# Performance work log

Measured on AMD Instinct MI355X. Metric: run time of the kernel, lower is better.

The kernel has to match this reference:

```python
import jax, jax.numpy as jnp
import numpy as np
from jax import lax

B, N, IN_DIM, OUT_DIM = 4, 8192, 32, 128
NPOINT, RADIUS, NSAMPLE = 1024, 0.2, 32
BN_EPS = 1e-5

def _sqdist(a, b):
    # a: [B,n,3], b: [B,m,3] -> [B,n,m] squared euclidean distances
    return (jnp.sum(a * a, -1)[:, :, None] + jnp.sum(b * b, -1)[:, None, :]
            - 2.0 * jnp.einsum('bnd,bmd->bnm', a, b))

def _fps(xyz, npoint):
    # farthest point sampling, sequential by nature -> lax.scan over npoint steps
    Bn, Np, _ = xyz.shape
    def step(carry, _):
        dist, far = carry
        centroid = jnp.take_along_axis(xyz, far[:, None, None], axis=1)  # [B,1,3]
        dist = jnp.minimum(dist, jnp.sum((xyz - centroid) ** 2, -1))
        return (dist, jnp.argmax(dist, -1).astype(jnp.int32)), far
    init = (jnp.full((Bn, Np), 1e10, xyz.dtype), jnp.zeros((Bn,), jnp.int32))
    _, idx = lax.scan(step, init, None, length=npoint)
    return idx.T  # [B, npoint]

def _gather_points(x, idx):  # x [B,N,D], idx [B,...] -> [B,...,D]
    return jax.vmap(lambda p, i: p[i])(x, idx)

def _gather_feats(f, idx):  # f [B,C,N], idx [B,...] -> [B,C,...]
    return jax.vmap(lambda p, i: p[:, i])(f, idx)

def _ball_query(new_xyz, xyz):
    d2 = _sqdist(new_xyz, xyz)  # [B,P,N]
    Np = xyz.shape[1]
    cand = jnp.where(d2 < RADIUS ** 2, jnp.arange(Np, dtype=jnp.int32), Np)
    idx = -lax.top_k(-cand, NSAMPLE)[0]  # first NSAMPLE in-radius indices (sorted)
    return jnp.where(idx == Np, idx[..., :1], idx)  # pad misses with first hit

def _bn(x, gamma, beta, axes):
    # training-mode batch norm over `axes`, channel axis = 1
    m = jnp.mean(x, axes, keepdims=True)
    v = jnp.var(x, axes, keepdims=True)
    sh = (1, -1) + (1,) * (x.ndim - 2)
    return (x - m) * (gamma.reshape(sh) / jnp.sqrt(v + BN_EPS)) + beta.reshape(sh)

def _forward(xyz, features, W_sa0, g_sa0, b_sa0, W_sa1, g_sa1, b_sa1, W_sa2, g_sa2, b_sa2,
             W_fp0, g_fp0, b_fp0, W_fp1, g_fp1, b_fp1,
             Wc1, bc1, g1, b1, Wc2, bc2, g2, b2, Wc3, bc3):
    # --- PointnetSAModuleVotes: FPS + ball query + group (use_xyz, normalize_xyz) + MLP + maxpool ---
    fps_idx = _fps(xyz, NPOINT)
    new_xyz = _gather_points(xyz, fps_idx)                           # [B,P,3]
    gidx = _ball_query(new_xyz, xyz)                                 # [B,P,S]
    gxyz = (_gather_points(xyz, gidx) - new_xyz[:, :, None, :]) / RADIUS  # centered, normalized
    h = jnp.concatenate([gxyz.transpose(0, 3, 1, 2), _gather_feats(features, gidx)], 1)  # [B,3+C,P,S]
    for W, g, b in ((W_sa0, g_sa0, b_sa0), (W_sa1, g_sa1, b_sa1), (W_sa2, g_sa2, b_sa2)):
        h = jax.nn.relu(_bn(jnp.einsum('oc,bcps->bops', W, h), g, b, (0, 2, 3)))
    feat_sa = jnp.max(h, -1)                                         # [B,128,P]
    # --- PointnetFPModule: 3-NN interpolation (inv-sq-dist weights) + skip concat + MLP ---
    d2 = _sqdist(xyz, new_xyz)                                       # [B,N,P]
    neg, idx3 = lax.top_k(-d2, 3)
    recip = 1.0 / (jnp.maximum(-neg, 0.0) + 1e-8)
    w = recip / jnp.sum(recip, -1, keepdims=True)                    # [B,N,3]
    interp = jnp.sum(_gather_feats(feat_sa, idx3) * w[:, None, :, :], -1)  # [B,128,N]
    h = jnp.concatenate([interp, features], 1)                       # [B,128+C,N]
    for W, g, b in ((W_fp0, g_fp0, b_fp0), (W_fp1, g_fp1, b_fp1)):
        h = jax.nn.relu(_bn(jnp.einsum('oc,bcn->bon', W, h), g, b, (0, 2)))
    seed_features = h                                                # [B,128,N]
    # --- vote head: conv1d(1) + BN + ReLU x2, then conv1d(1) -> [3 offset | 1 score | out_dim feat] ---
    net = jax.nn.relu(_bn(jnp.einsum('oc,bcn->bon', Wc1, seed_features) + bc1[:, None], g1, b1, (0, 2)))
    net = jax.nn.relu(_bn(jnp.einsum('oc,bcn->bon', Wc2, net) + bc2[:, None], g2, b2, (0, 2)))
    net = (jnp.einsum('oc,bcn->bon', Wc3, net) + bc3[:, None]).transpose(0, 2, 1)  # [B,N,4+out]
    offset = net[:, :, 0:3]
    vote_xyz = xyz + offset
    vote_scores = jax.nn.sigmoid(net[:, :, 3])
    vf = seed_features.transpose(0, 2, 1) + net[:, :, 4:]
    vote_features = vf / jnp.maximum(jnp.linalg.norm(vf, axis=2, keepdims=True), 1e-12)  # F.normalize
    return vote_xyz, offset, vote_scores, vote_features

def setup_inputs():
    key = jax.random.key(0)
    ks = jax.random.split(key, 40)
    he = lambda k, o, c: jax.random.normal(k, (o, c), jnp.float32) * float(np.sqrt(2.0 / c))
    inp = {'xyz': jax.random.uniform(ks[0], (B, N, 3), jnp.float32),
           'features': jax.random.normal(ks[1], (B, IN_DIM, N), jnp.float32)}
    j = 2
    dims_sa = [IN_DIM + 3, 128, 128, 128]  # use_xyz adds 3 to first layer
    for i in range(3):
        inp[f'W_sa{i}'] = he(ks[j], 128, dims_sa[i]); j += 1
        inp[f'g_sa{i}'] = 1.0 + 0.1 * jax.random.normal(ks[j], (128,), jnp.float32); j += 1
        inp[f'b_sa{i}'] = 0.1 * jax.random.normal(ks[j], (128,), jnp.float32); j += 1
    dims_fp = [IN_DIM + 128, 128, 128]
    for i in range(2):
        inp[f'W_fp{i}'] = he(ks[j], 128, dims_fp[i]); j += 1
        inp[f'g_fp{i}'] = 1.0 + 0.1 * jax.random.normal(ks[j], (128,), jnp.float32); j += 1
        inp[f'b_fp{i}'] = 0.1 * jax.random.normal(ks[j], (128,), jnp.float32); j += 1
    inp['Wc1'] = he(ks[j], 128, 128); j += 1
    inp['bc1'] = 0.01 * jax.random.normal(ks[j], (128,), jnp.float32); j += 1
    inp['g1'] = 1.0 + 0.1 * jax.random.normal(ks[j], (128,), jnp.float32); j += 1
    inp['b1'] = 0.1 * jax.random.normal(ks[j], (128,), jnp.float32); j += 1
    inp['Wc2'] = he(ks[j], 128, 128); j += 1
    inp['bc2'] = 0.01 * jax.random.normal(ks[j], (128,), jnp.float32); j += 1
    inp['g2'] = 1.0 + 0.1 * jax.random.normal(ks[j], (128,), jnp.float32); j += 1
    inp['b2'] = 0.1 * jax.random.normal(ks[j], (128,), jnp.float32); j += 1
    inp['Wc3'] = he(ks[j], 4 + OUT_DIM, 128); j += 1
    inp['bc3'] = 0.01 * jax.random.normal(ks[j], (4 + OUT_DIM,), jnp.float32); j += 1
    return inp

def reference(xyz, features, W_sa0, g_sa0, b_sa0, W_sa1, g_sa1, b_sa1, W_sa2, g_sa2, b_sa2,
              W_fp0, g_fp0, b_fp0, W_fp1, g_fp1, b_fp1,
              Wc1, bc1, g1, b1, Wc2, bc2, g2, b2, Wc3, bc3):
    return _forward(xyz, features, W_sa0, g_sa0, b_sa0, W_sa1, g_sa1, b_sa1, W_sa2, g_sa2, b_sa2,
                    W_fp0, g_fp0, b_fp0, W_fp1, g_fp1, b_fp1,
                    Wc1, bc1, g1, b1, Wc2, bc2, g2, b2, Wc3, bc3)
```

## Files before the change

kernel.cpp:

```cpp
#include <hip/hip_runtime.h>
#include <hip/hip_bf16.h>
#include <math.h>

namespace {

constexpr int BB  = 4;
constexpr int NN  = 8192;
constexpr int IND = 32;
constexpr int NPT = 1024;
constexpr int NSM = 32;
constexpr int SACOLS = BB * NPT * NSM;
constexpr int FPCOLS = BB * NN;
constexpr int CSTR = 132;

__device__ __forceinline__ double sqn3_f64(float x, float y, float z) {
#pragma clang fp contract(off)
    double dx = (double)x, dy = (double)y, dz = (double)z;
    return (dx * dx + dy * dy) + dz * dz;
}
__device__ __forceinline__ double dot3_f64(float ax, float ay, float az,
                                           float bx, float by, float bz) {
#pragma clang fp contract(off)
    return ((double)ax * (double)bx + (double)ay * (double)by) + (double)az * (double)bz;
}
__device__ __forceinline__ double sqd_f64(double sa, double sb, double dot) {
#pragma clang fp contract(off)
    return (sa + sb) - 2.0 * dot;
}

__global__ __launch_bounds__(256)
void k_fps(const float* __restrict__ xyz, float* __restrict__ new_xyz)
{
#pragma clang fp contract(off)
    const int b   = blockIdx.x;
    const int tid = threadIdx.x;
    const float* P = xyz + (size_t)b * NN * 3;

    __shared__ float sx[NN];
    __shared__ float sy[NN];
    __shared__ float sz[NN];
    __shared__ float ctrs[NPT * 3];
    __shared__ unsigned long long wv[2][4];

    float px[32], py[32], pz[32], dd[32];
#pragma unroll
    for (int i = 0; i < 32; ++i) {
        int p = tid + i * 256;
        float x = P[p * 3 + 0], y = P[p * 3 + 1], z = P[p * 3 + 2];
        px[i] = x; py[i] = y; pz[i] = z; dd[i] = 1e10f;
        sx[p] = x; sy[p] = y; sz[p] = z;
    }
    float cx = P[0], cy = P[1], cz = P[2];
    __syncthreads();

    for (int t = 0; t < NPT; ++t) {
        if (tid == 0) {
            ctrs[t * 3 + 0] = cx;
            ctrs[t * 3 + 1] = cy;
            ctrs[t * 3 + 2] = cz;
        }
        if (t == NPT - 1) break;

        unsigned long long best = 0ull;
#pragma unroll
        for (int i = 0; i < 32; ++i) {
            float dx = px[i] - cx;
            float dy = py[i] - cy;
            float dz = pz[i] - cz;
            float d  = (dx * dx + dy * dy) + dz * dz;
            float nd = fminf(dd[i], d);
            dd[i] = nd;
            unsigned int lo = (unsigned)(NN - 1) - (unsigned)(tid + i * 256);
            unsigned long long cand =
                ((unsigned long long)__float_as_uint(nd) << 32) | lo;
            best = (cand > best) ? cand : best;
        }
        for (int off = 32; off > 0; off >>= 1) {
            unsigned long long o = __shfl_down(best, off);
            best = (o > best) ? o : best;
        }
        const int buf = t & 1;
        if ((tid & 63) == 0) wv[buf][tid >> 6] = best;
        __syncthreads();
        unsigned long long w0 = wv[buf][0];
#pragma unroll
        for (int k = 1; k < 4; ++k) {
            unsigned long long wk = wv[buf][k];
            w0 = (wk > w0) ? wk : w0;
        }
        const int idx = (NN - 1) - (int)(unsigned)(w0 & 0xFFFFFFFFull);
        cx = sx[idx]; cy = sy[idx]; cz = sz[idx];
    }

    __syncthreads();
    float* O = new_xyz + (size_t)b * NPT * 3;
    for (int i = tid; i < NPT * 3; i += 256) O[i] = ctrs[i];
}

__global__ __launch_bounds__(256)
void k_ballquery(const float* __restrict__ xyz, const float* __restrict__ new_xyz,
                 int* __restrict__ gidx)
{
    const int wv   = threadIdx.x >> 6;
    const int lane = threadIdx.x & 63;
    const int cid  = blockIdx.x * 4 + wv;
    const int b    = cid >> 10;
    const float* P = xyz + (size_t)b * NN * 3;

    const float cx = new_xyz[(size_t)cid * 3 + 0];
    const float cy = new_xyz[(size_t)cid * 3 + 1];
    const float cz = new_xyz[(size_t)cid * 3 + 2];
    const double sa = sqn3_f64(cx, cy, cz);
    const double R2 = 0.2 * 0.2;

    int cnt = 0;
    int firstidx = -1;
    int* G = gidx + (size_t)cid * NSM;

    for (int base = 0; base < NN && cnt < NSM; base += 64) {
        int p = base + lane;
        float x = P[p * 3 + 0], y = P[p * 3 + 1], z = P[p * 3 + 2];
        double sb  = sqn3_f64(x, y, z);
        double dot = dot3_f64(cx, cy, cz, x, y, z);
        double d2  = sqd_f64(sa, sb, dot);
        bool hit = d2 < R2;
        unsigned long long m = __ballot(hit);
        if (firstidx < 0 && m != 0ull) firstidx = base + __builtin_ctzll(m);
        int before = __popcll(m & ((1ull << lane) - 1ull));
        int pos = cnt + before;
        if (hit && pos < NSM) G[pos] = p;
        cnt += __popcll(m);
    }
    if (firstidx < 0) firstidx = 0;
    if (cnt < NSM) {
        for (int j = cnt + lane; j < NSM; j += 64) G[j] = firstidx;
    }
}

__global__ __launch_bounds__(256)
void k_group(const float* __restrict__ xyz, const float* __restrict__ feats,
             const float* __restrict__ new_xyz, const int* __restrict__ gidx,
             float* __restrict__ h0)
{
    const int col = blockIdx.x * 256 + threadIdx.x;
    const int cid = col >> 5;
    const int b   = col >> 15;
    const int g   = gidx[col];
    const float* Pt = xyz + ((size_t)b * NN + g) * 3;
    const float* Ct = new_xyz + (size_t)cid * 3;
    h0[(size_t)0 * SACOLS + col] = __fsub_rn(Pt[0], Ct[0]) / 0.2f;
    h0[(size_t)1 * SACOLS + col] = __fsub_rn(Pt[1], Ct[1]) / 0.2f;
    h0[(size_t)2 * SACOLS + col] = __fsub_rn(Pt[2], Ct[2]) / 0.2f;
    const float* FT = feats + (size_t)b * IND * NN;
    for (int c = 0; c < IND; ++c)
        h0[(size_t)(3 + c) * SACOLS + col] = FT[(size_t)c * NN + g];
}

__global__ __launch_bounds__(256)
void k_conv(const float* __restrict__ X, const float* __restrict__ W,
            const float* __restrict__ bias,
            const float* __restrict__ scale, const float* __restrict__ shift,
            float* __restrict__ Z, int Cin, int Cout, int ncol, int apply_act)
{
    __shared__ __align__(16) float Xs[32][64];
    __shared__ float Ws[64][33];
    const int tid  = threadIdx.x;
    const int col0 = blockIdx.x * 64;
    const int o0   = blockIdx.y * 64;
    const int tx   = tid & 15;
    const int ty   = tid >> 4;
    float acc[4][4] = {};

    for (int kk = 0; kk < Cin; kk += 32) {
#pragma unroll
        for (int i = 0; i < 8; ++i) {
            int idx = tid + i * 256;
            int c = idx >> 6, cc = idx & 63;
            int ch = kk + c;
            float v = 0.0f;
            if (ch < Cin) {
                v = X[(size_t)ch * ncol + col0 + cc];
                if (apply_act) v = fmaxf(fmaf(v, scale[ch], shift[ch]), 0.0f);
            }
            Xs[c][cc] = v;
        }
#pragma unroll
        for (int i = 0; i < 8; ++i) {
            int idx = tid + i * 256;
            int o = idx >> 5, c = idx & 31;
            int ch = kk + c, oo = o0 + o;
            Ws[o][c] = (ch < Cin && oo < Cout) ? W[(size_t)oo * Cin + ch] : 0.0f;
        }
        __syncthreads();
#pragma unroll
        for (int c = 0; c < 32; ++c) {
            const float4 xv = *reinterpret_cast<const float4*>(&Xs[c][tx * 4]);
            float w0 = Ws[ty * 4 + 0][c];
            float w1 = Ws[ty * 4 + 1][c];
            float w2 = Ws[ty * 4 + 2][c];
            float w3 = Ws[ty * 4 + 3][c];
            acc[0][0] = fmaf(w0, xv.x, acc[0][0]); acc[0][1] = fmaf(w0, xv.y, acc[0][1]);
            acc[0][2] = fmaf(w0, xv.z, acc[0][2]); acc[0][3] = fmaf(w0, xv.w, acc[0][3]);
            acc[1][0] = fmaf(w1, xv.x, acc[1][0]); acc[1][1] = fmaf(w1, xv.y, acc[1][1]);
            acc[1][2] = fmaf(w1, xv.z, acc[1][2]); acc[1][3] = fmaf(w1, xv.w, acc[1][3]);
            acc[2][0] = fmaf(w2, xv.x, acc[2][0]); acc[2][1] = fmaf(w2, xv.y, acc[2][1]);
            acc[2][2] = fmaf(w2, xv.z, acc[2][2]); acc[2][3] = fmaf(w2, xv.w, acc[2][3]);
            acc[3][0] = fmaf(w3, xv.x, acc[3][0]); acc[3][1] = fmaf(w3, xv.y, acc[3][1]);
            acc[3][2] = fmaf(w3, xv.z, acc[3][2]); acc[3][3] = fmaf(w3, xv.w, acc[3][3]);
        }
        __syncthreads();
    }
#pragma unroll
    for (int i = 0; i < 4; ++i) {
        int o = o0 + ty * 4 + i;
        if (o >= Cout) break;
        float bz = bias ? bias[o] : 0.0f;
#pragma unroll
        for (int j = 0; j < 4; ++j)
            Z[(size_t)o * ncol + col0 + tx * 4 + j] = acc[i][j] + bz;
    }
}

__global__ __launch_bounds__(256)
void k_stats_partial(const float* __restrict__ Z, double* __restrict__ part, int ncol, int nb)
{
    const int c = blockIdx.x, blk = blockIdx.y;
    const int chunk = ncol / nb;
    const float* p = Z + (size_t)c * ncol + (size_t)blk * chunk;
    double s = 0.0, q = 0.0;
    for (int j = threadIdx.x; j < chunk; j += 256) { double v = (double)p[j]; s += v; q += v * v; }
    __shared__ double ss[256];
    __shared__ double qq[256];
    ss[threadIdx.x] = s; qq[threadIdx.x] = q;
    __syncthreads();
    for (int off = 128; off > 0; off >>= 1) {
        if (threadIdx.x < off) { ss[threadIdx.x] += ss[threadIdx.x + off]; qq[threadIdx.x] += qq[threadIdx.x + off]; }
        __syncthreads();
    }
    if (threadIdx.x == 0) {
        part[(size_t)(c * nb + blk) * 2 + 0] = ss[0];
        part[(size_t)(c * nb + blk) * 2 + 1] = qq[0];
    }
}

__global__ void k_stats_final(const double* __restrict__ part,
                              const float* __restrict__ gamma, const float* __restrict__ beta,
                              float* __restrict__ sc_out, float* __restrict__ sh_out,
                              int C, int nb, double n)
{
    int c = threadIdx.x;
    if (c >= C) return;
    double s = 0.0, q = 0.0;
    for (int i = 0; i < nb; ++i) {
        s += part[(size_t)(c * nb + i) * 2 + 0];
        q += part[(size_t)(c * nb + i) * 2 + 1];
    }
    double mean = s / n;
    double var  = q / n - mean * mean;
    double scl  = (double)gamma[c] / sqrt(var + 1e-5);
    sc_out[c] = (float)scl;
    sh_out[c] = (float)((double)beta[c] - mean * scl);
}

__global__ __launch_bounds__(256)
void k_maxpool(const float* __restrict__ Z, const float* __restrict__ sc,
               const float* __restrict__ sh, float* __restrict__ feat)
{
    const int idx = blockIdx.x * 256 + threadIdx.x;
    const int bp  = idx & 4095;
    const int c   = idx >> 12;
    const float s = sc[c], h = sh[c];
    const float* p = Z + (size_t)c * SACOLS + (size_t)bp * 32;
    float m = 0.0f;
    for (int ss = 0; ss < 32; ++ss) m = fmaxf(m, fmaxf(fmaf(p[ss], s, h), 0.0f));
    feat[(size_t)c * (BB * NPT) + bp] = m;
}

__global__ __launch_bounds__(256)
void k_3nn(const float* __restrict__ xyz, const float* __restrict__ new_xyz,
           int* __restrict__ idx3, float* __restrict__ w3)
{
    const int gid = blockIdx.x * 256 + threadIdx.x;
    const int b = gid >> 13;
    __shared__ float  cxs[NPT];
    __shared__ float  cys[NPT];
    __shared__ float  czs[NPT];
    __shared__ double cns[NPT];
    const float* C = new_xyz + (size_t)b * NPT * 3;
    for (int i = threadIdx.x; i < NPT; i += 256) {
        float x = C[i * 3], y = C[i * 3 + 1], z = C[i * 3 + 2];
        cxs[i] = x; cys[i] = y; czs[i] = z; cns[i] = sqn3_f64(x, y, z);
    }
    __syncthreads();

    const float* P = xyz + (size_t)gid * 3;
    const float px = P[0], py = P[1], pz = P[2];
    const double sb = sqn3_f64(px, py, pz);
    double d0 = 1e30, d1 = 1e30, d2v = 1e30;
    int    i0 = 0, i1 = 0, i2 = 0;
    for (int m = 0; m < NPT; ++m) {
        double dot = dot3_f64(px, py, pz, cxs[m], cys[m], czs[m]);
        double d   = sqd_f64(sb, cns[m], dot);
        if (d < d0)       { d2v = d1; i2 = i1; d1 = d0; i1 = i0; d0 = d; i0 = m; }
        else if (d < d1)  { d2v = d1; i2 = i1; d1 = d;  i1 = m; }
        else if (d < d2v) { d2v = d;  i2 = m; }
    }
    {
#pragma clang fp contract(off)
        double e0 = fmax(d0, 0.0), e1 = fmax(d1, 0.0), e2 = fmax(d2v, 0.0);
        double r0 = 1.0 / (e0 + 1e-8);
        double r1 = 1.0 / (e1 + 1e-8);
        double r2 = 1.0 / (e2 + 1e-8);
        double rs = (r0 + r1) + r2;
        idx3[(size_t)gid * 3 + 0] = i0; idx3[(size_t)gid * 3 + 1] = i1; idx3[(size_t)gid * 3 + 2] = i2;
        w3[(size_t)gid * 3 + 0] = (float)(r0 / rs);
        w3[(size_t)gid * 3 + 1] = (float)(r1 / rs);
        w3[(size_t)gid * 3 + 2] = (float)(r2 / rs);
    }
}

__global__ __launch_bounds__(256)
void k_hfp(const float* __restrict__ feats, const float* __restrict__ feat_sa,
           const int* __restrict__ idx3, const float* __restrict__ w3,
           float* __restrict__ hfp)
{
    const int col = blockIdx.x * 256 + threadIdx.x;
    const int b = col >> 13, n = col & 8191;
    const int ia = idx3[(size_t)col * 3 + 0];
    const int ib = idx3[(size_t)col * 3 + 1];
    const int ic = idx3[(size_t)col * 3 + 2];
    const float wa = w3[(size_t)col * 3 + 0];
    const float wb = w3[(size_t)col * 3 + 1];
    const float wc = w3[(size_t)col * 3 + 2];
    const int cb = b * NPT;
    for (int o = 0; o < 128; ++o) {
        const float* f = feat_sa + (size_t)o * (BB * NPT) + cb;
        hfp[(size_t)o * FPCOLS + col] = f[ia] * wa + f[ib] * wb + f[ic] * wc;
    }
    const float* FT = feats + (size_t)b * IND * NN;
    for (int c = 0; c < IND; ++c)
        hfp[(size_t)(128 + c) * FPCOLS + col] = FT[(size_t)c * NN + n];
}

__global__ __launch_bounds__(256)
void k_outputs(const float* __restrict__ xyz, const float* __restrict__ Zc3,
               const float* __restrict__ Zf1, const float* __restrict__ sc4,
               const float* __restrict__ sh4, float* __restrict__ out)
{
    const int col = blockIdx.x * 256 + threadIdx.x;
    const float n0 = Zc3[(size_t)0 * FPCOLS + col];
    const float n1 = Zc3[(size_t)1 * FPCOLS + col];
    const float n2 = Zc3[(size_t)2 * FPCOLS + col];
    const float n3 = Zc3[(size_t)3 * FPCOLS + col];
    const float* P = xyz + (size_t)col * 3;

    float* o_vxyz = out;
    float* o_off  = out + 98304;
    float* o_sc   = out + 196608;
    float* o_vf   = out + 229376;

    o_off[(size_t)col * 3 + 0] = n0;
    o_off[(size_t)col * 3 + 1] = n1;
    o_off[(size_t)col * 3 + 2] = n2;
    o_vxyz[(size_t)col * 3 + 0] = __fadd_rn(P[0], n0);
    o_vxyz[(size_t)col * 3 + 1] = __fadd_rn(P[1], n1);
    o_vxyz[(size_t)col * 3 + 2] = __fadd_rn(P[2], n2);
    o_sc[col] = 1.0f / (1.0f + expf(-n3));

    float sumsq = 0.0f;
    for (int c = 0; c < 128; ++c) {
        float seed = fmaxf(fmaf(Zf1[(size_t)c * FPCOLS + col], sc4[c], sh4[c]), 0.0f);
        float v = seed + Zc3[(size_t)(4 + c) * FPCOLS + col];
        sumsq = fmaf(v, v, sumsq);
    }
    float inv = 1.0f / fmaxf(sqrtf(sumsq), 1e-12f);
    for (int c = 0; c < 128; ++c) {
        float seed = fmaxf(fmaf(Zf1[(size_t)c * FPCOLS + col], sc4[c], sh4[c]), 0.0f);
        float v = seed + Zc3[(size_t)(4 + c) * FPCOLS + col];
        o_vf[(size_t)col * 128 + c] = v * inv;
    }
}

__global__ void k_sentinel(float* out)
{
    if (threadIdx.x < 8) out[threadIdx.x] = 12345.0f;
}

}

extern "C" void kernel_launch(void* const* d_in, const int* in_sizes, int n_in,
                              void* d_out, int out_size, void* d_ws, size_t ws_size,
                              hipStream_t stream)
{
    (void)in_sizes; (void)n_in; (void)out_size;
    const float* xyz   = (const float*)d_in[0];
    const float* feats = (const float*)d_in[1];
    const float* W_sa0 = (const float*)d_in[2];
    const float* g_sa0 = (const float*)d_in[3];
    const float* b_sa0 = (const float*)d_in[4];
    const float* W_sa1 = (const float*)d_in[5];
    const float* g_sa1 = (const float*)d_in[6];
    const float* b_sa1 = (const float*)d_in[7];
    const float* W_sa2 = (const float*)d_in[8];
    const float* g_sa2 = (const float*)d_in[9];
    const float* b_sa2 = (const float*)d_in[10];
    const float* W_fp0 = (const float*)d_in[11];
    const float* g_fp0 = (const float*)d_in[12];
    const float* b_fp0 = (const float*)d_in[13];
    const float* W_fp1 = (const float*)d_in[14];
    const float* g_fp1 = (const float*)d_in[15];
    const float* b_fp1 = (const float*)d_in[16];
    const float* Wc1   = (const float*)d_in[17];
    const float* bc1   = (const float*)d_in[18];
    const float* g1    = (const float*)d_in[19];
    const float* b1    = (const float*)d_in[20];
    const float* Wc2   = (const float*)d_in[21];
    const float* bc2   = (const float*)d_in[22];
    const float* g2    = (const float*)d_in[23];
    const float* b2    = (const float*)d_in[24];
    const float* Wc3   = (const float*)d_in[25];
    const float* bc3   = (const float*)d_in[26];

    char* ws = (char*)d_ws;
    size_t off = 0;
    auto alloc = [&](size_t bytes) -> size_t {
        size_t o = off;
        off += (bytes + 255) & ~(size_t)255;
        return o;
    };
    float*  new_xyz = (float*) (ws + alloc((size_t)BB * NPT * 3 * 4));
    int*    gidx    = (int*)   (ws + alloc((size_t)BB * NPT * NSM * 4));
    int*    idx3    = (int*)   (ws + alloc((size_t)FPCOLS * 3 * 4));
    float*  w3      = (float*) (ws + alloc((size_t)FPCOLS * 3 * 4));
    double* part    = (double*)(ws + alloc((size_t)132 * 32 * 2 * 8));
    float*  stats   = (float*) (ws + alloc((size_t)7 * 2 * CSTR * 4));
    float*  regA    = (float*) (ws + alloc((size_t)35 * SACOLS * 4));
    float*  ZA      = (float*) (ws + alloc((size_t)128 * SACOLS * 4));
    float*  ZB      = (float*) (ws + alloc((size_t)128 * SACOLS * 4));
    float*  feat_sa = (float*) (ws + alloc((size_t)128 * BB * NPT * 4));
    size_t required = off;

    if (ws_size < required) {
        k_sentinel<<<1, 64, 0, stream>>>((float*)d_out);
        return;
    }

    float* h0  = regA;
    float* Zc3 = regA;
    float* hfp = ZA;
    float* Zf0 = ZA + (size_t)160 * FPCOLS;
    float* Zc1 = ZA + (size_t)(160 + 128) * FPCOLS;
    float* Zf1 = ZB;
    float* Zc2 = ZB + (size_t)128 * FPCOLS;

    float* st[7];
    for (int l = 0; l < 7; ++l) st[l] = stats + (size_t)l * 2 * CSTR;
    const double nSA = (double)SACOLS, nFP = (double)FPCOLS;

    k_fps<<<BB, 256, 0, stream>>>(xyz, new_xyz);
    k_ballquery<<<(BB * NPT) / 4, 256, 0, stream>>>(xyz, new_xyz, gidx);
    k_group<<<SACOLS / 256, 256, 0, stream>>>(xyz, feats, new_xyz, gidx, h0);

    k_conv<<<dim3(SACOLS / 64, 2), 256, 0, stream>>>(h0, W_sa0, nullptr, nullptr, nullptr, ZA, 35, 128, SACOLS, 0);
    k_stats_partial<<<dim3(128, 32), 256, 0, stream>>>(ZA, part, SACOLS, 32);
    k_stats_final<<<1, 256, 0, stream>>>(part, g_sa0, b_sa0, st[0], st[0] + CSTR, 128, 32, nSA);

    k_conv<<<dim3(SACOLS / 64, 2), 256, 0, stream>>>(ZA, W_sa1, nullptr, st[0], st[0] + CSTR, ZB, 128, 128, SACOLS, 1);
    k_stats_partial<<<dim3(128, 32), 256, 0, stream>>>(ZB, part, SACOLS, 32);
    k_stats_final<<<1, 256, 0, stream>>>(part, g_sa1, b_sa1, st[1], st[1] + CSTR, 128, 32, nSA);

    k_conv<<<dim3(SACOLS / 64, 2), 256, 0, stream>>>(ZB, W_sa2, nullptr, st[1], st[1] + CSTR, ZA, 128, 128, SACOLS, 1);
    k_stats_partial<<<dim3(128, 32), 256, 0, stream>>>(ZA, part, SACOLS, 32);
    k_stats_final<<<1, 256, 0, stream>>>(part, g_sa2, b_sa2, st[2], st[2] + CSTR, 128, 32, nSA);

    k_maxpool<<<(128 * BB * NPT) / 256, 256, 0, stream>>>(ZA, st[2], st[2] + CSTR, feat_sa);

    k_3nn<<<FPCOLS / 256, 256, 0, stream>>>(xyz, new_xyz, idx3, w3);
    k_hfp<<<FPCOLS / 256, 256, 0, stream>>>(feats, feat_sa, idx3, w3, hfp);

    k_conv<<<dim3(FPCOLS / 64, 2), 256, 0, stream>>>(hfp, W_fp0, nullptr, nullptr, nullptr, Zf0, 160, 128, FPCOLS, 0);
    k_stats_partial<<<dim3(128, 32), 256, 0, stream>>>(Zf0, part, FPCOLS, 32);
    k_stats_final<<<1, 256, 0, stream>>>(part, g_fp0, b_fp0, st[3], st[3] + CSTR, 128, 32, nFP);

    k_conv<<<dim3(FPCOLS / 64, 2), 256, 0, stream>>>(Zf0, W_fp1, nullptr, st[3], st[3] + CSTR, Zf1, 128, 128, FPCOLS, 1);
    k_stats_partial<<<dim3(128, 32), 256, 0, stream>>>(Zf1, part, FPCOLS, 32);
    k_stats_final<<<1, 256, 0, stream>>>(part, g_fp1, b_fp1, st[4], st[4] + CSTR, 128, 32, nFP);

    k_conv<<<dim3(FPCOLS / 64, 2), 256, 0, stream>>>(Zf1, Wc1, bc1, st[4], st[4] + CSTR, Zc1, 128, 128, FPCOLS, 1);
    k_stats_partial<<<dim3(128, 32), 256, 0, stream>>>(Zc1, part, FPCOLS, 32);
    k_stats_final<<<1, 256, 0, stream>>>(part, g1, b1, st[5], st[5] + CSTR, 128, 32, nFP);

    k_conv<<<dim3(FPCOLS / 64, 2), 256, 0, stream>>>(Zc1, Wc2, bc2, st[5], st[5] + CSTR, Zc2, 128, 128, FPCOLS, 1);
    k_stats_partial<<<dim3(128, 32), 256, 0, stream>>>(Zc2, part, FPCOLS, 32);
    k_stats_final<<<1, 256, 0, stream>>>(part, g2, b2, st[6], st[6] + CSTR, 128, 32, nFP);

    k_conv<<<dim3(FPCOLS / 64, 3), 256, 0, stream>>>(Zc2, Wc3, bc3, st[6], st[6] + CSTR, Zc3, 128, 132, FPCOLS, 1);

    k_outputs<<<FPCOLS / 256, 256, 0, stream>>>(xyz, Zc3, Zf1, st[4], st[4] + CSTR, (float*)d_out);
}
```

Baseline: 2.175 ms.

## Fuse batch-norm statistics into conv epilogue and simplify FPS argmax

Drops the separate k_stats_partial pass. Each conv block now computes per-channel sum and sum-of-squares in double over its 64 columns, reduces them with warp shuffles and writes one partial per block. This saves a full re-read of each activation tensor from global memory. The cost is that k_stats_final, still a single 256-thread block, must now sum up to 2048 partials per channel with only two threads per channel, which may be slow. The FPS loop also tracks a per-thread float max and index and packs the 64-bit key once, instead of doing a 64-bit compare per point.

```diff
diff --git a/kernel.cpp b/kernel.cpp
--- a/kernel.cpp
+++ b/kernel.cpp
@@ -61,7 +61,8 @@
         }
         if (t == NPT - 1) break;
 
-        unsigned long long best = 0ull;
+        float bv = -1.0f;
+        int   bi = 0;
 #pragma unroll
         for (int i = 0; i < 32; ++i) {
             float dx = px[i] - cx;
@@ -70,11 +71,11 @@
             float d  = (dx * dx + dy * dy) + dz * dz;
             float nd = fminf(dd[i], d);
             dd[i] = nd;
-            unsigned int lo = (unsigned)(NN - 1) - (unsigned)(tid + i * 256);
-            unsigned long long cand =
-                ((unsigned long long)__float_as_uint(nd) << 32) | lo;
-            best = (cand > best) ? cand : best;
-        }
+            if (nd > bv) { bv = nd; bi = i; }
+        }
+        unsigned long long best =
+            ((unsigned long long)__float_as_uint(bv) << 32) |
+            (unsigned)(NN - 1 - (tid + bi * 256));
         for (int off = 32; off > 0; off >>= 1) {
             unsigned long long o = __shfl_down(best, off);
             best = (o > best) ? o : best;
@@ -160,7 +161,8 @@
 void k_conv(const float* __restrict__ X, const float* __restrict__ W,
             const float* __restrict__ bias,
             const float* __restrict__ scale, const float* __restrict__ shift,
-            float* __restrict__ Z, int Cin, int Cout, int ncol, int apply_act)
+            float* __restrict__ Z, double* __restrict__ part,
+            int Cin, int Cout, int ncol, int apply_act)
 {
     __shared__ __align__(16) float Xs[32][64];
     __shared__ float Ws[64][33];
@@ -215,51 +217,53 @@
         int o = o0 + ty * 4 + i;
         if (o >= Cout) break;
         float bz = bias ? bias[o] : 0.0f;
-#pragma unroll
-        for (int j = 0; j < 4; ++j)
-            Z[(size_t)o * ncol + col0 + tx * 4 + j] = acc[i][j] + bz;
-    }
-}
-
-__global__ __launch_bounds__(256)
-void k_stats_partial(const float* __restrict__ Z, double* __restrict__ part, int ncol, int nb)
-{
-    const int c = blockIdx.x, blk = blockIdx.y;
-    const int chunk = ncol / nb;
-    const float* p = Z + (size_t)c * ncol + (size_t)blk * chunk;
-    double s = 0.0, q = 0.0;
-    for (int j = threadIdx.x; j < chunk; j += 256) { double v = (double)p[j]; s += v; q += v * v; }
-    __shared__ double ss[256];
-    __shared__ double qq[256];
-    ss[threadIdx.x] = s; qq[threadIdx.x] = q;
-    __syncthreads();
-    for (int off = 128; off > 0; off >>= 1) {
-        if (threadIdx.x < off) { ss[threadIdx.x] += ss[threadIdx.x + off]; qq[threadIdx.x] += qq[threadIdx.x + off]; }
-        __syncthreads();
-    }
-    if (threadIdx.x == 0) {
-        part[(size_t)(c * nb + blk) * 2 + 0] = ss[0];
-        part[(size_t)(c * nb + blk) * 2 + 1] = qq[0];
+        float v0 = acc[i][0] + bz;
+        float v1 = acc[i][1] + bz;
+        float v2 = acc[i][2] + bz;
+        float v3 = acc[i][3] + bz;
+        float* zp = Z + (size_t)o * ncol + col0 + tx * 4;
+        zp[0] = v0; zp[1] = v1; zp[2] = v2; zp[3] = v3;
+
+        if (part) {
+            double s = ((double)v0 + (double)v1) + ((double)v2 + (double)v3);
+            double q = ((double)v0 * v0 + (double)v1 * v1)
+                     + ((double)v2 * v2 + (double)v3 * v3);
+            for (int off = 8; off > 0; off >>= 1) {
+                s += __shfl_down(s, off);
+                q += __shfl_down(q, off);
+            }
+            if (tx == 0) {
+                const int nblk = ncol >> 6;
+                part[((size_t)o * nblk + blockIdx.x) * 2 + 0] = s;
+                part[((size_t)o * nblk + blockIdx.x) * 2 + 1] = q;
+            }
+        }
     }
 }
 
 __global__ void k_stats_final(const double* __restrict__ part,
                               const float* __restrict__ gamma, const float* __restrict__ beta,
                               float* __restrict__ sc_out, float* __restrict__ sh_out,
-                              int C, int nb, double n)
-{
-    int c = threadIdx.x;
+                              int C, int nblk, double n)
+{
+    const int t = threadIdx.x;
+    const int c = t >> 1;
+    const int h = t & 1;
     if (c >= C) return;
+    const int half = nblk >> 1;
+    const double* p = part + ((size_t)c * nblk + (size_t)h * half) * 2;
     double s = 0.0, q = 0.0;
-    for (int i = 0; i < nb; ++i) {
-        s += part[(size_t)(c * nb + i) * 2 + 0];
-        q += part[(size_t)(c * nb + i) * 2 + 1];
-    }
-    double mean = s / n;
-    double var  = q / n - mean * mean;
-    double scl  = (double)gamma[c] / sqrt(var + 1e-5);
-    sc_out[c] = (float)scl;
-    sh_out[c] = (float)((double)beta[c] - mean * scl);
+    for (int i = 0; i < half; ++i) { s += p[i * 2 + 0]; q += p[i * 2 + 1]; }
+    double so = __shfl_down(s, 1);
+    double qo = __shfl_down(q, 1);
+    if (h == 0) {
+        s += so; q += qo;
+        double mean = s / n;
+        double var  = q / n - mean * mean;
+        double scl  = (double)gamma[c] / sqrt(var + 1e-5);
+        sc_out[c] = (float)scl;
+        sh_out[c] = (float)((double)beta[c] - mean * scl);
+    }
 }
 
 __global__ __launch_bounds__(256)
@@ -432,7 +436,7 @@
     int*    gidx    = (int*)   (ws + alloc((size_t)BB * NPT * NSM * 4));
     int*    idx3    = (int*)   (ws + alloc((size_t)FPCOLS * 3 * 4));
     float*  w3      = (float*) (ws + alloc((size_t)FPCOLS * 3 * 4));
-    double* part    = (double*)(ws + alloc((size_t)132 * 32 * 2 * 8));
+    double* part    = (double*)(ws + alloc((size_t)128 * 2048 * 2 * 8));
     float*  stats   = (float*) (ws + alloc((size_t)7 * 2 * CSTR * 4));
     float*  regA    = (float*) (ws + alloc((size_t)35 * SACOLS * 4));
     float*  ZA      = (float*) (ws + alloc((size_t)128 * SACOLS * 4));
@@ -456,45 +460,40 @@
     float* st[7];
     for (int l = 0; l < 7; ++l) st[l] = stats + (size_t)l * 2 * CSTR;
     const double nSA = (double)SACOLS, nFP = (double)FPCOLS;
+    const int nbSA = SACOLS / 64;
+    const int nbFP = FPCOLS / 64;
 
     k_fps<<<BB, 256, 0, stream>>>(xyz, new_xyz);
     k_ballquery<<<(BB * NPT) / 4, 256, 0, stream>>>(xyz, new_xyz, gidx);
     k_group<<<SACOLS / 256, 256, 0, stream>>>(xyz, feats, new_xyz, gidx, h0);
 
-    k_conv<<<dim3(SACOLS / 64, 2), 256, 0, stream>>>(h0, W_sa0, nullptr, nullptr, nullptr, ZA, 35, 128, SACOLS, 0);
-    k_stats_partial<<<dim3(128, 32), 256, 0, stream>>>(ZA, part, SACOLS, 32);
-    k_stats_final<<<1, 256, 0, stream>>>(part, g_sa0, b_sa0, st[0], st[0] + CSTR, 128, 32, nSA);
-
-    k_conv<<<dim3(SACOLS / 64, 2), 256, 0, stream>>>(ZA, W_sa1, nullptr, st[0], st[0] + CSTR, ZB, 128, 128, SACOLS, 1);
-    k_stats_partial<<<dim3(128, 32), 256, 0, stream>>>(ZB, part, SACOLS, 32);
-    k_stats_final<<<1, 256, 0, stream>>>(part, g_sa1, b_sa1, st[1], st[1] + CSTR, 128, 32, nSA);
-
-    k_conv<<<dim3(SACOLS / 64, 2), 256, 0, stream>>>(ZB, W_sa2, nullptr, st[1], st[1] + CSTR, ZA, 128, 128, SACOLS, 1);
-    k_stats_partial<<<dim3(128, 32), 256, 0, stream>>>(ZA, part, SACOLS, 32);
-    k_stats_final<<<1, 256, 0, stream>>>(part, g_sa2, b_sa2, st[2], st[2] + CSTR, 128, 32, nSA);
+    k_conv<<<dim3(SACOLS / 64, 2), 256, 0, stream>>>(h0, W_sa0, nullptr, nullptr, nullptr, ZA, part, 35, 128, SACOLS, 0);
+    k_stats_final<<<1, 256, 0, stream>>>(part, g_sa0, b_sa0, st[0], st[0] + CSTR, 128, nbSA, nSA);
+
+    k_conv<<<dim3(SACOLS / 64, 2), 256, 0, stream>>>(ZA, W_sa1, nullptr, st[0], st[0] + CSTR, ZB, part, 128, 128, SACOLS, 1);
+    k_stats_final<<<1, 256, 0, stream>>>(part, g_sa1, b_sa1, st[1], st[1] + CSTR, 128, nbSA, nSA);
+
+    k_conv<<<dim3(SACOLS / 64, 2), 256, 0, stream>>>(ZB, W_sa2, nullptr, st[1], st[1] + CSTR, ZA, part, 128, 128, SACOLS, 1);
+    k_stats_final<<<1, 256, 0, stream>>>(part, g_sa2, b_sa2, st[2], st[2] + CSTR, 128, nbSA, nSA);
 
     k_maxpool<<<(128 * BB * NPT) / 256, 256, 0, stream>>>(ZA, st[2], st[2] + CSTR, feat_sa);
 
     k_3nn<<<FPCOLS / 256, 256, 0, stream>>>(xyz, new_xyz, idx3, w3);
     k_hfp<<<FPCOLS / 256, 256, 0, stream>>>(feats, feat_sa, idx3, w3, hfp);
 
-    k_conv<<<dim3(FPCOLS / 64, 2), 256, 0, stream>>>(hfp, W_fp0, nullptr, nullptr, nullptr, Zf0, 160, 128, FPCOLS, 0);
-    k_stats_partial<<<dim3(128, 32), 256, 0, stream>>>(Zf0, part, FPCOLS, 32);
-    k_stats_final<<<1, 256, 0, stream>>>(part, g_fp0, b_fp0, st[3], st[3] + CSTR, 128, 32, nFP);
-
-    k_conv<<<dim3(FPCOLS / 64, 2), 256, 0, stream>>>(Zf0, W_fp1, nullptr, st[3], st[3] + CSTR, Zf1, 128, 128, FPCOLS, 1);
-    k_stats_partial<<<dim3(128, 32), 256, 0, stream>>>(Zf1, part, FPCOLS, 32);
-    k_stats_final<<<1, 256, 0, stream>>>(part, g_fp1, b_fp1, st[4], st[4] + CSTR, 128, 32, nFP);
-
-    k_conv<<<dim3(FPCOLS / 64, 2), 256, 0, stream>>>(Zf1, Wc1, bc1, st[4], st[4] + CSTR, Zc1, 128, 128, FPCOLS, 1);
-    k_stats_partial<<<dim3(128, 32), 256, 0, stream>>>(Zc1, part, FPCOLS, 32);
-    k_stats_final<<<1, 256, 0, stream>>>(part, g1, b1, st[5], st[5] + CSTR, 128, 32, nFP);
-
-    k_conv<<<dim3(FPCOLS / 64, 2), 256, 0, stream>>>(Zc1, Wc2, bc2, st[5], st[5] + CSTR, Zc2, 128, 128, FPCOLS, 1);
-    k_stats_partial<<<dim3(128, 32), 256, 0, stream>>>(Zc2, part, FPCOLS, 32);
-    k_stats_final<<<1, 256, 0, stream>>>(part, g2, b2, st[6], st[6] + CSTR, 128, 32, nFP);
-
-    k_conv<<<dim3(FPCOLS / 64, 3), 256, 0, stream>>>(Zc2, Wc3, bc3, st[6], st[6] + CSTR, Zc3, 128, 132, FPCOLS, 1);
+    k_conv<<<dim3(FPCOLS / 64, 2), 256, 0, stream>>>(hfp, W_fp0, nullptr, nullptr, nullptr, Zf0, part, 160, 128, FPCOLS, 0);
+    k_stats_final<<<1, 256, 0, stream>>>(part, g_fp0, b_fp0, st[3], st[3] + CSTR, 128, nbFP, nFP);
+
+    k_conv<<<dim3(FPCOLS / 64, 2), 256, 0, stream>>>(Zf0, W_fp1, nullptr, st[3], st[3] + CSTR, Zf1, part, 128, 128, FPCOLS, 1);
+    k_stats_final<<<1, 256, 0, stream>>>(part, g_fp1, b_fp1, st[4], st[4] + CSTR, 128, nbFP, nFP);
+
+    k_conv<<<dim3(FPCOLS / 64, 2), 256, 0, stream>>>(Zf1, Wc1, bc1, st[4], st[4] + CSTR, Zc1, part, 128, 128, FPCOLS, 1);
+    k_stats_final<<<1, 256, 0, stream>>>(part, g1, b1, st[5], st[5] + CSTR, 128, nbFP, nFP);
+
+    k_conv<<<dim3(FPCOLS / 64, 2), 256, 0, stream>>>(Zc1, Wc2, bc2, st[5], st[5] + CSTR, Zc2, part, 128, 128, FPCOLS, 1);
+    k_stats_final<<<1, 256, 0, stream>>>(part, g2, b2, st[6], st[6] + CSTR, 128, nbFP, nFP);
+
+    k_conv<<<dim3(FPCOLS / 64, 3), 256, 0, stream>>>(Zc2, Wc3, bc3, st[6], st[6] + CSTR, Zc3, nullptr, 128, 132, FPCOLS, 1);
 
     k_outputs<<<FPCOLS / 256, 256, 0, stream>>>(xyz, Zc3, Zf1, st[4], st[4] + CSTR, (float*)d_out);
 }
```

New measurement: 2.706 ms. 24.4% more time.
